# Performance work log

Hardware: AMD Instinct MI355X
Metric: run time of the kernel (lower is better)

The kernel has to match this reference:

```python
import jax, jax.numpy as jnp
import numpy as np
import math

D_MODEL = 4096
N_EXPERTS = 64
TOP_K = 2
CAPACITY_FACTOR = 1.2
N_TOKENS = 16384


def setup_inputs() -> dict:
    key = jax.random.key(0)
    k1, k2, k3 = jax.random.split(key, 3)
    x = jax.random.normal(k1, (N_TOKENS, D_MODEL), dtype=jnp.float32)
    W = jax.random.normal(k2, (N_EXPERTS, D_MODEL), dtype=jnp.float32) * (1.0 / math.sqrt(D_MODEL))
    b = jax.random.normal(k3, (N_EXPERTS,), dtype=jnp.float32) * 0.01
    return {"x": x, "W": W, "b": b, "training": 0}


def _route(x, W, b):
    # router linear: [N, d] @ [d, E] + [E]
    logits = x @ W.T + b
    # eval path: no gaussian gate noise (training=False)
    probs = jax.nn.softmax(logits, axis=-1)  # [N, E]
    topk_gates, topk_ids = jax.lax.top_k(probs, TOP_K)  # [N, K]
    N = x.shape[0]
    cap = int(math.ceil(CAPACITY_FACTOR * N / N_EXPERTS))

    flat_ids = topk_ids.reshape(-1)      # [N*K] int32
    flat_gates = topk_gates.reshape(-1)  # [N*K]
    M = flat_ids.shape[0]

    # Vectorized Switch-style capacity drop: sort slots by (expert asc, gate desc),
    # keep the first `cap` slots of each expert group. Replaces the per-expert
    # nonzero/argsort Python loop with a single sort + segment scan.
    order = jnp.lexsort((-flat_gates, flat_ids))  # primary key: expert id
    sorted_ids = flat_ids[order]
    counts = jax.ops.segment_sum(jnp.ones_like(flat_ids), flat_ids, num_segments=N_EXPERTS)
    starts = jnp.cumsum(counts) - counts          # first sorted index of each expert
    rank_in_expert = jnp.arange(M, dtype=counts.dtype) - starts[sorted_ids]
    keep_sorted = rank_in_expert < cap
    keep = jnp.zeros((M,), dtype=bool).at[order].set(keep_sorted)

    # aux load-balancing loss (Switch): importance x load
    importance = probs.sum(axis=0)  # [E]
    load = jax.ops.segment_sum(keep.astype(probs.dtype), flat_ids, num_segments=N_EXPERTS)
    Nf = float(N)
    aux_loss = (N_EXPERTS * (importance / Nf) * (load / Nf)).sum()

    mask = keep.reshape(N, TOP_K)
    return topk_ids, topk_gates, aux_loss, mask


def reference(x, W, b, training):
    # training == 0 -> noiseless gating, matching the deterministic eval path
    return _route(x, W, b)
```

## Files before the change

kernel.cpp:

```cpp
#include <hip/hip_runtime.h>
#include <math.h>

#define N_TOKENS  16384
#define D_MODEL   4096
#define N_EXPERTS 64
#define CAPACITY  308
#define BUCKET_CAP 1024
#define CAP_SLICES 4

#define NK     4
#define KSPLIT (D_MODEL / NK)
#define KTILE  64
#define NITER  (KSPLIT / KTILE)

typedef __attribute__((ext_vector_type(8))) short bf16x8;
typedef __attribute__((ext_vector_type(4))) float f32x4;

__device__ __forceinline__ unsigned short bf16_rne(float f) {
    unsigned u = __float_as_uint(f);
    u += 0x7fffu + ((u >> 16) & 1u);
    return (unsigned short)(u >> 16);
}
__device__ __forceinline__ float bf16_to_f32(unsigned short h) {
    return __uint_as_float(((unsigned)h) << 16);
}
__device__ __forceinline__ void split3(float f, unsigned short& h,
                                       unsigned short& m, unsigned short& l) {
    h = bf16_rne(f);
    float r1 = f - bf16_to_f32(h);
    m = bf16_rne(r1);
    float r2 = r1 - bf16_to_f32(m);
    l = bf16_rne(r2);
}

__device__ __forceinline__ void glds16(const void* g, void* l) {
    __builtin_amdgcn_global_load_lds(
        (const __attribute__((address_space(1))) void*)g,
        (__attribute__((address_space(3))) void*)l, 16, 0, 0);
}

__global__ __launch_bounds__(256) void wsplit_kernel(
    const float* __restrict__ W,
    unsigned short* __restrict__ whi, unsigned short* __restrict__ wmid,
    unsigned short* __restrict__ wlo)
{
    int i = (blockIdx.x * 256 + threadIdx.x) * 4;
    float4 w = *(const float4*)&W[i];
    float e[4] = {w.x, w.y, w.z, w.w};
    ushort4 h, m, l;
    unsigned short* hp = &h.x; unsigned short* mp = &m.x; unsigned short* lp = &l.x;
    #pragma unroll
    for (int j = 0; j < 4; j++) split3(e[j], hp[j], mp[j], lp[j]);
    *(ushort4*)&whi[i]  = h;
    *(ushort4*)&wmid[i] = m;
    *(ushort4*)&wlo[i]  = l;
}

__global__ __launch_bounds__(256, 4) void gemm_kernel(
    const float* __restrict__ x,
    const unsigned short* __restrict__ whi,
    const unsigned short* __restrict__ wmid,
    const unsigned short* __restrict__ wlo,
    float* __restrict__ part)
{
    __shared__ float          xs[64 * 64];
    __shared__ unsigned short bsh[64 * 64];
    __shared__ unsigned short bsm[64 * 64];
    __shared__ unsigned short bsl[64 * 64];

    const int tid   = threadIdx.x;
    const int lane  = tid & 63;
    const int wv    = tid >> 6;
    const int tg    = blockIdx.x & 255;
    const int nk    = blockIdx.x >> 8;
    const int tbase = tg * 64;
    const int kbase = nk * KSPLIT;

    const int xsub = lane >> 4;
    const int brow = lane >> 3;
    const int bcs  = (lane & 7) ^ brow;

    const int arow = lane & 15;
    const int akq  = lane >> 4;
    const int r7   = arow & 7;

    f32x4 acc[4];
    #pragma unroll
    for (int nt = 0; nt < 4; nt++)
        #pragma unroll
        for (int r = 0; r < 4; r++) acc[nt][r] = 0.f;

    for (int t = 0; t < NITER; t++) {
        const int kc = t * KTILE;

        #pragma unroll
        for (int m = 0; m < 4; m++) {
            int i   = wv + 4 * m;
            int row = 4 * i + xsub;
            int cs  = (lane & 15) ^ (row & 7);
            glds16(&x[(size_t)(tbase + row) * D_MODEL + kbase + kc + cs * 4],
                   &xs[i * 256]);
        }
        #pragma unroll
        for (int m = 0; m < 2; m++) {
            int j = wv + 4 * m;
            size_t soff = (size_t)(8 * j + brow) * D_MODEL + kbase + kc + bcs * 8;
            glds16(&whi [soff], &bsh[j * 512]);
            glds16(&wmid[soff], &bsm[j * 512]);
            glds16(&wlo [soff], &bsl[j * 512]);
        }
        __syncthreads();

        #pragma unroll
        for (int s = 0; s < 2; s++) {
            const float* xrow = &xs[(wv * 16 + arow) * 64];
            int c0 = (s * 8 + akq * 2)     ^ r7;
            int c1 = (s * 8 + akq * 2 + 1) ^ r7;
            float4 v0 = *(const float4*)&xrow[c0 * 4];
            float4 v1 = *(const float4*)&xrow[c1 * 4];
            float f[8] = {v0.x, v0.y, v0.z, v0.w, v1.x, v1.y, v1.z, v1.w};
            bf16x8 ahi, ami, alo;
            #pragma unroll
            for (int j = 0; j < 8; j++) {
                unsigned short h, m, l;
                split3(f[j], h, m, l);
                ahi[j] = (short)h; ami[j] = (short)m; alo[j] = (short)l;
            }
            int cb = s * 4 + akq;
            #pragma unroll
            for (int nt = 0; nt < 4; nt++) {
                int boff = (nt * 16 + arow) * 64 + ((cb ^ r7) * 8);
                bf16x8 bh = *(const bf16x8*)&bsh[boff];
                bf16x8 bm = *(const bf16x8*)&bsm[boff];
                bf16x8 bl = *(const bf16x8*)&bsl[boff];
                acc[nt] = __builtin_amdgcn_mfma_f32_16x16x32_bf16(ahi, bh, acc[nt], 0, 0, 0);
                acc[nt] = __builtin_amdgcn_mfma_f32_16x16x32_bf16(ahi, bm, acc[nt], 0, 0, 0);
                acc[nt] = __builtin_amdgcn_mfma_f32_16x16x32_bf16(ami, bh, acc[nt], 0, 0, 0);
                acc[nt] = __builtin_amdgcn_mfma_f32_16x16x32_bf16(ahi, bl, acc[nt], 0, 0, 0);
                acc[nt] = __builtin_amdgcn_mfma_f32_16x16x32_bf16(ami, bm, acc[nt], 0, 0, 0);
                acc[nt] = __builtin_amdgcn_mfma_f32_16x16x32_bf16(alo, bh, acc[nt], 0, 0, 0);
            }
        }
        __syncthreads();
    }

    #pragma unroll
    for (int nt = 0; nt < 4; nt++) {
        #pragma unroll
        for (int r = 0; r < 4; r++) {
            int tok = tbase + wv * 16 + akq * 4 + r;
            part[((size_t)nk * N_TOKENS + tok) * N_EXPERTS + nt * 16 + arow] = acc[nt][r];
        }
    }
}

__global__ __launch_bounds__(256) void topk_kernel(
    const float* __restrict__ part, const float* __restrict__ b,
    float* __restrict__ out_ids, float* __restrict__ out_gates,
    int* __restrict__ cnt, float* __restrict__ imp,
    float2* __restrict__ bucket, int bucket_cap,
    float* __restrict__ out_mask)
{
    __shared__ float imp_s[4][N_EXPERTS];
    __shared__ float res_g[4][16];
    __shared__ int   res_i[4][16];
    const int tid  = threadIdx.x;
    const int wave = tid >> 6;
    const int lane = tid & 63;
    const int tok0 = blockIdx.x * 32 + wave * 8;
    float impacc = 0.f;

    for (int j = 0; j < 8; j++) {
        int tok = tok0 + j;
        float v = b[lane];
        #pragma unroll
        for (int k = 0; k < NK; k++)
            v += part[((size_t)k * N_TOKENS + tok) * N_EXPERTS + lane];

        float m = v;
        #pragma unroll
        for (int s = 32; s > 0; s >>= 1) m = fmaxf(m, __shfl_xor(m, s));
        float p = expf(v - m);
        float sum = p;
        #pragma unroll
        for (int s = 32; s > 0; s >>= 1) sum += __shfl_xor(sum, s);
        float prob = p / sum;
        impacc += prob;

        float bp = prob; int bi = lane;
        #pragma unroll
        for (int s = 32; s > 0; s >>= 1) {
            float op = __shfl_xor(bp, s); int oi = __shfl_xor(bi, s);
            if (op > bp || (op == bp && oi < bi)) { bp = op; bi = oi; }
        }
        float p2 = (lane == bi) ? -1.f : prob;
        float bp2 = p2; int bi2 = lane;
        #pragma unroll
        for (int s = 32; s > 0; s >>= 1) {
            float op = __shfl_xor(bp2, s); int oi = __shfl_xor(bi2, s);
            if (op > bp2 || (op == bp2 && oi < bi2)) { bp2 = op; bi2 = oi; }
        }

        if (lane == 0) {
            res_g[wave][j * 2]     = bp;  res_i[wave][j * 2]     = bi;
            res_g[wave][j * 2 + 1] = bp2; res_i[wave][j * 2 + 1] = bi2;
        }
    }

    __builtin_amdgcn_wave_barrier();
    if (lane < 16) {
        int tok  = tok0 + (lane >> 1);
        int slot = tok * 2 + (lane & 1);
        float g  = res_g[wave][lane];
        int   id = res_i[wave][lane];
        out_ids[slot]   = (float)id;
        out_gates[slot] = g;
        int pos = atomicAdd(&cnt[id], 1);
        if (pos < bucket_cap)
            bucket[id * bucket_cap + pos] = make_float2(g, __int_as_float(slot));
        else
            out_mask[slot] = 0.f;
    }

    imp_s[wave][lane] = impacc;
    __syncthreads();
    if (wave == 0) {
        float s = imp_s[0][lane] + imp_s[1][lane] + imp_s[2][lane] + imp_s[3][lane];
        atomicAdd(&imp[lane], s);
    }
}

__global__ __launch_bounds__(256) void capacity_kernel(
    const int* __restrict__ cnt, const float2* __restrict__ bucket,
    float* __restrict__ out_mask, int bucket_cap)
{
    __shared__ __align__(16) float g_s[BUCKET_CAP];
    __shared__ __align__(16) int   i_s[BUCKET_CAP];
    const int e     = blockIdx.x / CAP_SLICES;
    const int slice = blockIdx.x % CAP_SLICES;
    int n = cnt[e];
    if (n > bucket_cap) n = bucket_cap;

    for (int i = threadIdx.x; i < n; i += 256) {
        float2 r = bucket[e * bucket_cap + i];
        g_s[i] = r.x;
        i_s[i] = __float_as_int(r.y);
    }
    __syncthreads();

    const int chunk = (n + CAP_SLICES - 1) / CAP_SLICES;
    const int i = slice * chunk + threadIdx.x;
    if (threadIdx.x < chunk && i < n) {
        const float gi = g_s[i];
        const int   ii = i_s[i];
        int rank = 0;
        const int n4 = n & ~3;
        for (int j = 0; j < n4; j += 4) {
            float4 g = *(const float4*)&g_s[j];
            int4   d = *(const int4*)&i_s[j];
            rank += (g.x > gi || (g.x == gi && d.x < ii)) ? 1 : 0;
            rank += (g.y > gi || (g.y == gi && d.y < ii)) ? 1 : 0;
            rank += (g.z > gi || (g.z == gi && d.z < ii)) ? 1 : 0;
            rank += (g.w > gi || (g.w == gi && d.w < ii)) ? 1 : 0;
        }
        for (int j = n4; j < n; j++) {
            float gj = g_s[j]; int ij = i_s[j];
            rank += (gj > gi || (gj == gi && ij < ii)) ? 1 : 0;
        }
        out_mask[ii] = (rank < CAPACITY) ? 1.f : 0.f;
    }
}

__global__ void aux_kernel(const int* __restrict__ cnt,
                           const float* __restrict__ imp,
                           float* __restrict__ out_aux)
{
    int lane = threadIdx.x;
    float load = (float)min(cnt[lane], CAPACITY);
    float v = (float)N_EXPERTS * (imp[lane] / (float)N_TOKENS) * (load / (float)N_TOKENS);
    #pragma unroll
    for (int s = 32; s > 0; s >>= 1) v += __shfl_xor(v, s);
    if (lane == 0) out_aux[0] = v;
}

extern "C" void kernel_launch(void* const* d_in, const int* in_sizes, int n_in,
                              void* d_out, int out_size, void* d_ws, size_t ws_size,
                              hipStream_t stream) {
    const float* x = (const float*)d_in[0];
    const float* W = (const float*)d_in[1];
    const float* b = (const float*)d_in[2];

    float* out       = (float*)d_out;
    float* out_ids   = out;
    float* out_gates = out + 32768;
    float* out_aux   = out + 65536;
    float* out_mask  = out + 65537;

    const size_t partN = (size_t)N_TOKENS * N_EXPERTS * sizeof(float);
    const size_t wN    = (size_t)N_EXPERTS * D_MODEL * sizeof(unsigned short);

    int*            cnt    = (int*)d_ws;
    float*          imp    = (float*)((char*)d_ws + 256);
    float*          part   = (float*)((char*)d_ws + 512);
    unsigned short* whi    = (unsigned short*)((char*)d_ws + 512 + NK * partN);
    unsigned short* wmid   = (unsigned short*)((char*)d_ws + 512 + NK * partN + wN);
    unsigned short* wlo    = (unsigned short*)((char*)d_ws + 512 + NK * partN + 2 * wN);
    float2*         bucket = (float2*)((char*)d_ws + 512 + NK * partN + 3 * wN);

    size_t used = 512 + NK * partN + 3 * wN;
    int bucket_cap = (ws_size > used) ? (int)((ws_size - used) / (N_EXPERTS * sizeof(float2))) : 0;
    if (bucket_cap > BUCKET_CAP) bucket_cap = BUCKET_CAP;

    hipMemsetAsync(d_ws, 0, 512, stream);

    wsplit_kernel<<<(N_EXPERTS * D_MODEL) / (256 * 4), 256, 0, stream>>>(W, whi, wmid, wlo);
    gemm_kernel<<<256 * NK, 256, 0, stream>>>(x, whi, wmid, wlo, part);
    topk_kernel<<<512, 256, 0, stream>>>(part, b, out_ids, out_gates,
                                         cnt, imp, bucket, bucket_cap, out_mask);
    capacity_kernel<<<N_EXPERTS * CAP_SLICES, 256, 0, stream>>>(cnt, bucket, out_mask, bucket_cap);
    aux_kernel<<<1, 64, 0, stream>>>(cnt, imp, out_aux);
}
```

Baseline: 504.7 us.

## Double token tile per GEMM block and use packed bf16 conversion for splits

The router GEMM block now covers 128 tokens instead of 64, with each wave computing two 16-row M sub-tiles, so every W tile loaded into LDS is reused twice and W traffic is halved. The fp32-to-3xbf16 split of x now uses the packed v_cvt_pk_bf16_f32 instruction on pairs, cutting the VALU work that competes with the MFMAs. In exchange the block uses more LDS and registers, launch bounds drop to 2 blocks per CU, and the grid halves to 512 blocks, which may leave the GPU underfilled and reduce latency hiding.

```diff
diff --git a/kernel.cpp b/kernel.cpp
--- a/kernel.cpp
+++ b/kernel.cpp
@@ -15,6 +15,7 @@
 
 typedef __attribute__((ext_vector_type(8))) short bf16x8;
 typedef __attribute__((ext_vector_type(4))) float f32x4;
+typedef __attribute__((ext_vector_type(4))) unsigned int u32x4;
 
 __device__ __forceinline__ unsigned short bf16_rne(float f) {
     unsigned u = __float_as_uint(f);
@@ -31,6 +32,23 @@
     m = bf16_rne(r1);
     float r2 = r1 - bf16_to_f32(m);
     l = bf16_rne(r2);
+}
+
+__device__ __forceinline__ unsigned cvt_pk_bf16(float a, float b) {
+    unsigned r;
+    asm("v_cvt_pk_bf16_f32 %0, %1, %2" : "=v"(r) : "v"(a), "v"(b));
+    return r;
+}
+__device__ __forceinline__ void split3_pk(float f0, float f1,
+                                          unsigned& hp, unsigned& mp, unsigned& lp) {
+    hp = cvt_pk_bf16(f0, f1);
+    float h0 = __uint_as_float(hp << 16);
+    float h1 = __uint_as_float(hp & 0xffff0000u);
+    float r0 = f0 - h0, r1 = f1 - h1;
+    mp = cvt_pk_bf16(r0, r1);
+    float m0 = __uint_as_float(mp << 16);
+    float m1 = __uint_as_float(mp & 0xffff0000u);
+    lp = cvt_pk_bf16(r0 - m0, r1 - m1);
 }
 
 __device__ __forceinline__ void glds16(const void* g, void* l) {
@@ -56,14 +74,14 @@
     *(ushort4*)&wlo[i]  = l;
 }
 
-__global__ __launch_bounds__(256, 4) void gemm_kernel(
+__global__ __launch_bounds__(256, 2) void gemm_kernel(
     const float* __restrict__ x,
     const unsigned short* __restrict__ whi,
     const unsigned short* __restrict__ wmid,
     const unsigned short* __restrict__ wlo,
     float* __restrict__ part)
 {
-    __shared__ float          xs[64 * 64];
+    __shared__ float          xs[128 * 64];
     __shared__ unsigned short bsh[64 * 64];
     __shared__ unsigned short bsm[64 * 64];
     __shared__ unsigned short bsl[64 * 64];
@@ -71,9 +89,9 @@
     const int tid   = threadIdx.x;
     const int lane  = tid & 63;
     const int wv    = tid >> 6;
-    const int tg    = blockIdx.x & 255;
-    const int nk    = blockIdx.x >> 8;
-    const int tbase = tg * 64;
+    const int tg    = blockIdx.x & 127;
+    const int nk    = blockIdx.x >> 7;
+    const int tbase = tg * 128;
     const int kbase = nk * KSPLIT;
 
     const int xsub = lane >> 4;
@@ -84,17 +102,19 @@
     const int akq  = lane >> 4;
     const int r7   = arow & 7;
 
-    f32x4 acc[4];
+    f32x4 acc[4][2];
     #pragma unroll
     for (int nt = 0; nt < 4; nt++)
         #pragma unroll
-        for (int r = 0; r < 4; r++) acc[nt][r] = 0.f;
+        for (int m2 = 0; m2 < 2; m2++)
+            #pragma unroll
+            for (int r = 0; r < 4; r++) acc[nt][m2][r] = 0.f;
 
     for (int t = 0; t < NITER; t++) {
         const int kc = t * KTILE;
 
         #pragma unroll
-        for (int m = 0; m < 4; m++) {
+        for (int m = 0; m < 8; m++) {
             int i   = wv + 4 * m;
             int row = 4 * i + xsub;
             int cs  = (lane & 15) ^ (row & 7);
@@ -113,45 +133,53 @@
 
         #pragma unroll
         for (int s = 0; s < 2; s++) {
-            const float* xrow = &xs[(wv * 16 + arow) * 64];
-            int c0 = (s * 8 + akq * 2)     ^ r7;
-            int c1 = (s * 8 + akq * 2 + 1) ^ r7;
-            float4 v0 = *(const float4*)&xrow[c0 * 4];
-            float4 v1 = *(const float4*)&xrow[c1 * 4];
-            float f[8] = {v0.x, v0.y, v0.z, v0.w, v1.x, v1.y, v1.z, v1.w};
-            bf16x8 ahi, ami, alo;
+            const int c0 = (s * 8 + akq * 2)     ^ r7;
+            const int c1 = (s * 8 + akq * 2 + 1) ^ r7;
+            unsigned ah[2][4], am[2][4], al[2][4];
             #pragma unroll
-            for (int j = 0; j < 8; j++) {
-                unsigned short h, m, l;
-                split3(f[j], h, m, l);
-                ahi[j] = (short)h; ami[j] = (short)m; alo[j] = (short)l;
+            for (int m2 = 0; m2 < 2; m2++) {
+                const float* xrow = &xs[(wv * 32 + m2 * 16 + arow) * 64];
+                float4 v0 = *(const float4*)&xrow[c0 * 4];
+                float4 v1 = *(const float4*)&xrow[c1 * 4];
+                split3_pk(v0.x, v0.y, ah[m2][0], am[m2][0], al[m2][0]);
+                split3_pk(v0.z, v0.w, ah[m2][1], am[m2][1], al[m2][1]);
+                split3_pk(v1.x, v1.y, ah[m2][2], am[m2][2], al[m2][2]);
+                split3_pk(v1.z, v1.w, ah[m2][3], am[m2][3], al[m2][3]);
             }
-            int cb = s * 4 + akq;
+            const int cb = (s * 4 + akq) ^ r7;
             #pragma unroll
             for (int nt = 0; nt < 4; nt++) {
-                int boff = (nt * 16 + arow) * 64 + ((cb ^ r7) * 8);
+                int boff = (nt * 16 + arow) * 64 + cb * 8;
                 bf16x8 bh = *(const bf16x8*)&bsh[boff];
                 bf16x8 bm = *(const bf16x8*)&bsm[boff];
                 bf16x8 bl = *(const bf16x8*)&bsl[boff];
-                acc[nt] = __builtin_amdgcn_mfma_f32_16x16x32_bf16(ahi, bh, acc[nt], 0, 0, 0);
-                acc[nt] = __builtin_amdgcn_mfma_f32_16x16x32_bf16(ahi, bm, acc[nt], 0, 0, 0);
-                acc[nt] = __builtin_amdgcn_mfma_f32_16x16x32_bf16(ami, bh, acc[nt], 0, 0, 0);
-                acc[nt] = __builtin_amdgcn_mfma_f32_16x16x32_bf16(ahi, bl, acc[nt], 0, 0, 0);
-                acc[nt] = __builtin_amdgcn_mfma_f32_16x16x32_bf16(ami, bm, acc[nt], 0, 0, 0);
-                acc[nt] = __builtin_amdgcn_mfma_f32_16x16x32_bf16(alo, bh, acc[nt], 0, 0, 0);
+                #pragma unroll
+                for (int m2 = 0; m2 < 2; m2++) {
+                    union { u32x4 u; bf16x8 v; } Ah, Am, Al;
+                    Ah.u = (u32x4){ah[m2][0], ah[m2][1], ah[m2][2], ah[m2][3]};
+                    Am.u = (u32x4){am[m2][0], am[m2][1], am[m2][2], am[m2][3]};
+                    Al.u = (u32x4){al[m2][0], al[m2][1], al[m2][2], al[m2][3]};
+                    acc[nt][m2] = __builtin_amdgcn_mfma_f32_16x16x32_bf16(Ah.v, bh, acc[nt][m2], 0, 0, 0);
+                    acc[nt][m2] = __builtin_amdgcn_mfma_f32_16x16x32_bf16(Ah.v, bm, acc[nt][m2], 0, 0, 0);
+                    acc[nt][m2] = __builtin_amdgcn_mfma_f32_16x16x32_bf16(Am.v, bh, acc[nt][m2], 0, 0, 0);
+                    acc[nt][m2] = __builtin_amdgcn_mfma_f32_16x16x32_bf16(Ah.v, bl, acc[nt][m2], 0, 0, 0);
+                    acc[nt][m2] = __builtin_amdgcn_mfma_f32_16x16x32_bf16(Am.v, bm, acc[nt][m2], 0, 0, 0);
+                    acc[nt][m2] = __builtin_amdgcn_mfma_f32_16x16x32_bf16(Al.v, bh, acc[nt][m2], 0, 0, 0);
+                }
             }
         }
         __syncthreads();
     }
 
     #pragma unroll
-    for (int nt = 0; nt < 4; nt++) {
-        #pragma unroll
-        for (int r = 0; r < 4; r++) {
-            int tok = tbase + wv * 16 + akq * 4 + r;
-            part[((size_t)nk * N_TOKENS + tok) * N_EXPERTS + nt * 16 + arow] = acc[nt][r];
-        }
-    }
+    for (int nt = 0; nt < 4; nt++)
+        #pragma unroll
+        for (int m2 = 0; m2 < 2; m2++)
+            #pragma unroll
+            for (int r = 0; r < 4; r++) {
+                int tok = tbase + wv * 32 + m2 * 16 + akq * 4 + r;
+                part[((size_t)nk * N_TOKENS + tok) * N_EXPERTS + nt * 16 + arow] = acc[nt][m2][r];
+            }
 }
 
 __global__ __launch_bounds__(256) void topk_kernel(
@@ -314,7 +342,7 @@
     hipMemsetAsync(d_ws, 0, 512, stream);
 
     wsplit_kernel<<<(N_EXPERTS * D_MODEL) / (256 * 4), 256, 0, stream>>>(W, whi, wmid, wlo);
-    gemm_kernel<<<256 * NK, 256, 0, stream>>>(x, whi, wmid, wlo, part);
+    gemm_kernel<<<128 * NK, 256, 0, stream>>>(x, whi, wmid, wlo, part);
     topk_kernel<<<512, 256, 0, stream>>>(part, b, out_ids, out_gates,
                                          cnt, imp, bucket, bucket_cap, out_mask);
     capacity_kernel<<<N_EXPERTS * CAP_SLICES, 256, 0, stream>>>(cnt, bucket, out_mask, bucket_cap);
```

Result: no change. 506.4 us (+0.4%).

## Double-buffer GEMM LDS tiles, use packed bf16 conversion, fold aux into capacity kernel

Applied to the files above, without the earlier changes.

The router GEMM now stages the next K tile into a second LDS buffer while computing on the current one, removing one barrier per iteration. The three-way bf16 split of x uses the packed v_cvt_pk_bf16_f32 instruction to cut conversion ALU work. The aux-loss reduction moves into an extra block of the capacity kernel, saving a launch. Doubling LDS lowers occupancy to two blocks per CU, trading latency hiding for overlap.

```diff
diff --git a/kernel.cpp b/kernel.cpp
--- a/kernel.cpp
+++ b/kernel.cpp
@@ -15,6 +15,7 @@
 
 typedef __attribute__((ext_vector_type(8))) short bf16x8;
 typedef __attribute__((ext_vector_type(4))) float f32x4;
+typedef __attribute__((ext_vector_type(4))) unsigned int u32x4;
 
 __device__ __forceinline__ unsigned short bf16_rne(float f) {
     unsigned u = __float_as_uint(f);
@@ -31,6 +32,23 @@
     m = bf16_rne(r1);
     float r2 = r1 - bf16_to_f32(m);
     l = bf16_rne(r2);
+}
+
+__device__ __forceinline__ unsigned cvt_pk_bf16(float a, float b) {
+    unsigned r;
+    asm("v_cvt_pk_bf16_f32 %0, %1, %2" : "=v"(r) : "v"(a), "v"(b));
+    return r;
+}
+__device__ __forceinline__ void split3_pk(float f0, float f1,
+                                          unsigned& hp, unsigned& mp, unsigned& lp) {
+    hp = cvt_pk_bf16(f0, f1);
+    float h0 = __uint_as_float(hp << 16);
+    float h1 = __uint_as_float(hp & 0xffff0000u);
+    float r0 = f0 - h0, r1 = f1 - h1;
+    mp = cvt_pk_bf16(r0, r1);
+    float m0 = __uint_as_float(mp << 16);
+    float m1 = __uint_as_float(mp & 0xffff0000u);
+    lp = cvt_pk_bf16(r0 - m0, r1 - m1);
 }
 
 __device__ __forceinline__ void glds16(const void* g, void* l) {
@@ -56,17 +74,17 @@
     *(ushort4*)&wlo[i]  = l;
 }
 
-__global__ __launch_bounds__(256, 4) void gemm_kernel(
+__global__ __launch_bounds__(256, 2) void gemm_kernel(
     const float* __restrict__ x,
     const unsigned short* __restrict__ whi,
     const unsigned short* __restrict__ wmid,
     const unsigned short* __restrict__ wlo,
     float* __restrict__ part)
 {
-    __shared__ float          xs[64 * 64];
-    __shared__ unsigned short bsh[64 * 64];
-    __shared__ unsigned short bsm[64 * 64];
-    __shared__ unsigned short bsl[64 * 64];
+    __shared__ float          xs[2][64 * 64];
+    __shared__ unsigned short bsh[2][64 * 64];
+    __shared__ unsigned short bsm[2][64 * 64];
+    __shared__ unsigned short bsl[2][64 * 64];
 
     const int tid   = threadIdx.x;
     const int lane  = tid & 63;
@@ -84,63 +102,71 @@
     const int akq  = lane >> 4;
     const int r7   = arow & 7;
 
-    f32x4 acc[4];
-    #pragma unroll
-    for (int nt = 0; nt < 4; nt++)
-        #pragma unroll
-        for (int r = 0; r < 4; r++) acc[nt][r] = 0.f;
-
-    for (int t = 0; t < NITER; t++) {
-        const int kc = t * KTILE;
-
+    auto stage = [&](int buf, int kc) {
         #pragma unroll
         for (int m = 0; m < 4; m++) {
             int i   = wv + 4 * m;
             int row = 4 * i + xsub;
             int cs  = (lane & 15) ^ (row & 7);
             glds16(&x[(size_t)(tbase + row) * D_MODEL + kbase + kc + cs * 4],
-                   &xs[i * 256]);
+                   &xs[buf][i * 256]);
         }
         #pragma unroll
         for (int m = 0; m < 2; m++) {
             int j = wv + 4 * m;
             size_t soff = (size_t)(8 * j + brow) * D_MODEL + kbase + kc + bcs * 8;
-            glds16(&whi [soff], &bsh[j * 512]);
-            glds16(&wmid[soff], &bsm[j * 512]);
-            glds16(&wlo [soff], &bsl[j * 512]);
-        }
-        __syncthreads();
+            glds16(&whi [soff], &bsh[buf][j * 512]);
+            glds16(&wmid[soff], &bsm[buf][j * 512]);
+            glds16(&wlo [soff], &bsl[buf][j * 512]);
+        }
+    };
+
+    f32x4 acc[4];
+    #pragma unroll
+    for (int nt = 0; nt < 4; nt++)
+        #pragma unroll
+        for (int r = 0; r < 4; r++) acc[nt][r] = 0.f;
+
+    stage(0, 0);
+    __syncthreads();
+
+    for (int t = 0; t < NITER; t++) {
+        const int cur = t & 1;
+
+        if (t + 1 < NITER) stage(cur ^ 1, (t + 1) * KTILE);
 
         #pragma unroll
         for (int s = 0; s < 2; s++) {
-            const float* xrow = &xs[(wv * 16 + arow) * 64];
-            int c0 = (s * 8 + akq * 2)     ^ r7;
-            int c1 = (s * 8 + akq * 2 + 1) ^ r7;
+            const float* xrow = &xs[cur][(wv * 16 + arow) * 64];
+            const int c0 = (s * 8 + akq * 2)     ^ r7;
+            const int c1 = (s * 8 + akq * 2 + 1) ^ r7;
             float4 v0 = *(const float4*)&xrow[c0 * 4];
             float4 v1 = *(const float4*)&xrow[c1 * 4];
-            float f[8] = {v0.x, v0.y, v0.z, v0.w, v1.x, v1.y, v1.z, v1.w};
-            bf16x8 ahi, ami, alo;
-            #pragma unroll
-            for (int j = 0; j < 8; j++) {
-                unsigned short h, m, l;
-                split3(f[j], h, m, l);
-                ahi[j] = (short)h; ami[j] = (short)m; alo[j] = (short)l;
-            }
-            int cb = s * 4 + akq;
+            unsigned ah[4], am[4], al[4];
+            split3_pk(v0.x, v0.y, ah[0], am[0], al[0]);
+            split3_pk(v0.z, v0.w, ah[1], am[1], al[1]);
+            split3_pk(v1.x, v1.y, ah[2], am[2], al[2]);
+            split3_pk(v1.z, v1.w, ah[3], am[3], al[3]);
+            union { u32x4 u; bf16x8 v; } Ah, Am, Al;
+            Ah.u = (u32x4){ah[0], ah[1], ah[2], ah[3]};
+            Am.u = (u32x4){am[0], am[1], am[2], am[3]};
+            Al.u = (u32x4){al[0], al[1], al[2], al[3]};
+            const int cb = (s * 4 + akq) ^ r7;
             #pragma unroll
             for (int nt = 0; nt < 4; nt++) {
-                int boff = (nt * 16 + arow) * 64 + ((cb ^ r7) * 8);
-                bf16x8 bh = *(const bf16x8*)&bsh[boff];
-                bf16x8 bm = *(const bf16x8*)&bsm[boff];
-                bf16x8 bl = *(const bf16x8*)&bsl[boff];
-                acc[nt] = __builtin_amdgcn_mfma_f32_16x16x32_bf16(ahi, bh, acc[nt], 0, 0, 0);
-                acc[nt] = __builtin_amdgcn_mfma_f32_16x16x32_bf16(ahi, bm, acc[nt], 0, 0, 0);
-                acc[nt] = __builtin_amdgcn_mfma_f32_16x16x32_bf16(ami, bh, acc[nt], 0, 0, 0);
-                acc[nt] = __builtin_amdgcn_mfma_f32_16x16x32_bf16(ahi, bl, acc[nt], 0, 0, 0);
-                acc[nt] = __builtin_amdgcn_mfma_f32_16x16x32_bf16(ami, bm, acc[nt], 0, 0, 0);
-                acc[nt] = __builtin_amdgcn_mfma_f32_16x16x32_bf16(alo, bh, acc[nt], 0, 0, 0);
+                int boff = (nt * 16 + arow) * 64 + cb * 8;
+                bf16x8 bh = *(const bf16x8*)&bsh[cur][boff];
+                bf16x8 bm = *(const bf16x8*)&bsm[cur][boff];
+                bf16x8 bl = *(const bf16x8*)&bsl[cur][boff];
+                acc[nt] = __builtin_amdgcn_mfma_f32_16x16x32_bf16(Ah.v, bh, acc[nt], 0, 0, 0);
+                acc[nt] = __builtin_amdgcn_mfma_f32_16x16x32_bf16(Ah.v, bm, acc[nt], 0, 0, 0);
+                acc[nt] = __builtin_amdgcn_mfma_f32_16x16x32_bf16(Am.v, bh, acc[nt], 0, 0, 0);
+                acc[nt] = __builtin_amdgcn_mfma_f32_16x16x32_bf16(Ah.v, bl, acc[nt], 0, 0, 0);
+                acc[nt] = __builtin_amdgcn_mfma_f32_16x16x32_bf16(Am.v, bm, acc[nt], 0, 0, 0);
+                acc[nt] = __builtin_amdgcn_mfma_f32_16x16x32_bf16(Al.v, bh, acc[nt], 0, 0, 0);
             }
         }
+
         __syncthreads();
     }
 
@@ -232,10 +258,24 @@
 
 __global__ __launch_bounds__(256) void capacity_kernel(
     const int* __restrict__ cnt, const float2* __restrict__ bucket,
-    float* __restrict__ out_mask, int bucket_cap)
+    float* __restrict__ out_mask, int bucket_cap,
+    const float* __restrict__ imp, float* __restrict__ out_aux)
 {
     __shared__ __align__(16) float g_s[BUCKET_CAP];
     __shared__ __align__(16) int   i_s[BUCKET_CAP];
+
+    if (blockIdx.x == N_EXPERTS * CAP_SLICES) {
+        int lane = threadIdx.x;
+        if (lane < 64) {
+            float load = (float)min(cnt[lane], CAPACITY);
+            float v = (float)N_EXPERTS * (imp[lane] / (float)N_TOKENS) * (load / (float)N_TOKENS);
+            #pragma unroll
+            for (int s = 32; s > 0; s >>= 1) v += __shfl_xor(v, s);
+            if (lane == 0) out_aux[0] = v;
+        }
+        return;
+    }
+
     const int e     = blockIdx.x / CAP_SLICES;
     const int slice = blockIdx.x % CAP_SLICES;
     int n = cnt[e];
@@ -271,18 +311,6 @@
     }
 }
 
-__global__ void aux_kernel(const int* __restrict__ cnt,
-                           const float* __restrict__ imp,
-                           float* __restrict__ out_aux)
-{
-    int lane = threadIdx.x;
-    float load = (float)min(cnt[lane], CAPACITY);
-    float v = (float)N_EXPERTS * (imp[lane] / (float)N_TOKENS) * (load / (float)N_TOKENS);
-    #pragma unroll
-    for (int s = 32; s > 0; s >>= 1) v += __shfl_xor(v, s);
-    if (lane == 0) out_aux[0] = v;
-}
-
 extern "C" void kernel_launch(void* const* d_in, const int* in_sizes, int n_in,
                               void* d_out, int out_size, void* d_ws, size_t ws_size,
                               hipStream_t stream) {
@@ -317,6 +345,6 @@
     gemm_kernel<<<256 * NK, 256, 0, stream>>>(x, whi, wmid, wlo, part);
     topk_kernel<<<512, 256, 0, stream>>>(part, b, out_ids, out_gates,
                                          cnt, imp, bucket, bucket_cap, out_mask);
-    capacity_kernel<<<N_EXPERTS * CAP_SLICES, 256, 0, stream>>>(cnt, bucket, out_mask, bucket_cap);
-    aux_kernel<<<1, 64, 0, stream>>>(cnt, imp, out_aux);
-}
+    capacity_kernel<<<N_EXPERTS * CAP_SLICES + 1, 256, 0, stream>>>(
+        cnt, bucket, out_mask, bucket_cap, imp, out_aux);
+}
```

Result: no change. 503.0 us (-0.3%).
